# Kernel tuning notes

Hardware: AMD Instinct MI355X
Metric: run time of the kernel (lower is better)

## Reference

```python
import jax, jax.numpy as jnp
import numpy as np

B, S, D, H = 8, 1024, 512, 8
DK = D // H
NEG = -1e30  # stands in for -inf; masked probs are zero-filled afterwards, so math matches


def setup_inputs() -> dict:
    rng = jax.random.key(0)
    ks = jax.random.split(rng, 12)
    f = lambda k, shape: jax.random.normal(k, shape, dtype=jnp.float32)
    w = lambda k: f(k, (D, D)) * 0.02  # stored as (in, out); y = x @ W + b
    return {
        "query": f(ks[0], (B, S, D)),
        "key": f(ks[1], (B, S, D)),
        "value": f(ks[2], (B, S, D)),
        "mask": jax.random.randint(ks[3], (B, 1, S), 0, 2, dtype=jnp.int32),
        "Wq": w(ks[4]), "bq": jnp.zeros((D,), jnp.float32),
        "Wk": w(ks[5]), "bk": jnp.zeros((D,), jnp.float32),
        "Wv": w(ks[6]), "bv": jnp.zeros((D,), jnp.float32),
        "Wo": w(ks[7]), "bo": jnp.zeros((D,), jnp.float32),
    }


def reference(query, key, value, mask, Wq, bq, Wk, bk, Wv, bv, Wo, bo):
    # QKV projections -> (B, H, S, DK)
    def proj(x, W, b):
        return (x @ W + b).reshape(B, -1, H, DK).transpose(0, 2, 1, 3)

    q = proj(query, Wq, bq)
    k = proj(key, Wk, bk)
    v = proj(value, Wv, bv)

    scores = jnp.einsum("bhqd,bhkd->bhqk", q, k) / jnp.sqrt(jnp.float32(DK))
    m = (mask[:, None, :, :] == 0)  # (B, 1, 1, S): True where masked out
    scores = jnp.where(m, NEG, scores)
    attn = jax.nn.softmax(scores, axis=-1)
    attn = jnp.where(m, 0.0, attn)  # dropout rate is 0.0 -> identity

    x = jnp.einsum("bhqk,bhkd->bhqd", attn, v)
    x = x.transpose(0, 2, 1, 3).reshape(B, -1, D)  # (B, S, D)
    return x @ Wo + bo
```

## Files before the change

### kernel.cpp

```cpp
#include <hip/hip_runtime.h>
#include <hip/hip_bf16.h>

#define NB 8
#define NS 1024
#define ND 512
#define NH 8
#define NDK 64

typedef __attribute__((ext_vector_type(8))) short bf16x8;
typedef __attribute__((ext_vector_type(4))) float f32x4;
typedef __attribute__((ext_vector_type(16))) float f32x16;

#define QSCALE 0.18033688011112042f
#define NEGBIG -3.0e38f

#define CVTPK(dst, a, b) \
    asm("v_cvt_pk_bf16_f32 %0, %1, %2" : "=v"(dst) : "v"(a), "v"(b))
#define PLSWAP(a, b) \
    asm("v_permlane32_swap_b32 %0, %1" : "+v"(a), "+v"(b))

__device__ __forceinline__ unsigned short bfround(float f) {
    union { float f; unsigned u; } v; v.f = f;
    unsigned u = v.u;
    u += 0x7fffu + ((u >> 16) & 1u);
    return (unsigned short)(u >> 16);
}


__global__ __launch_bounds__(256) void wt_kernel(const float* __restrict__ W0,
                                                 const float* __restrict__ W1,
                                                 const float* __restrict__ W2,
                                                 const float* __restrict__ W3,
                                                 unsigned short* __restrict__ wt) {
    __shared__ float sh[64][65];
    const int z = blockIdx.z;
    const float* W = z == 0 ? W0 : z == 1 ? W1 : z == 2 ? W2 : W3;
    unsigned short* out = wt + (size_t)z * ND * ND;
    const int o0 = blockIdx.x * 64, i0 = blockIdx.y * 64;
    const int tx = threadIdx.x & 63;
    const int ty = threadIdx.x >> 6;
    #pragma unroll
    for (int rr = 0; rr < 16; ++rr) {
        const int row = ty * 16 + rr;
        sh[row][tx] = W[(size_t)(i0 + row) * ND + o0 + tx];
    }
    __syncthreads();
    #pragma unroll
    for (int rr = 0; rr < 16; ++rr) {
        const int row = ty * 16 + rr;
        out[(size_t)(o0 + row) * ND + i0 + tx] = bfround(sh[tx][row]);
    }
}

__global__ __launch_bounds__(256, 5) void gemm_qkv(
    const float* __restrict__ A0, const float* __restrict__ A1, const float* __restrict__ A2,
    const unsigned short* __restrict__ wt,
    const float* __restrict__ b0, const float* __restrict__ b1, const float* __restrict__ b2,
    unsigned short* __restrict__ outb) {
    __shared__ unsigned short SM[15360];
    const int t = threadIdx.x;
    const int lane = t & 63, w = t >> 6;
    const int wr = w >> 1, wc = w & 1;
    const int lr = lane & 15, lg = lane >> 4;
    const int bid = blockIdx.x;
    const int u = (bid & 7) * 192 + (bid >> 3);
    const int xt = u & 3, yt = (u >> 2) & 127, z = u >> 9;
    const float* A = z == 0 ? A0 : z == 1 ? A1 : A2;
    const float* bias = z == 0 ? b0 : z == 1 ? b1 : b2;
    const unsigned short* Wt = wt + (size_t)z * ND * ND;
    unsigned short* outp = outb + (size_t)z * NB * NH * NS * NDK;
    const int m0 = yt * 64, n0 = xt * 128;

    const int a_row = t >> 3;
    const int a_col = (t & 7) * 4;
    const int b_row = t >> 2;
    const int b_col = (t & 3) * 8;

    f32x4 acc[2][4];
    #pragma unroll
    for (int i = 0; i < 2; ++i)
        #pragma unroll
        for (int j = 0; j < 4; ++j) acc[i][j] = (f32x4){0.f, 0.f, 0.f, 0.f};

    f32x4 ra[2];
    bf16x8 rbv[2];

#define QKV_LOAD(kt) do {                                                      \
        const int _k0 = (kt) * 32;                                             \
        ra[0] = *(const f32x4*)(A + (size_t)(m0 + a_row) * ND + _k0 + a_col);  \
        ra[1] = *(const f32x4*)(A + (size_t)(m0 + a_row + 32) * ND + _k0 + a_col); \
        rbv[0] = *(const bf16x8*)(Wt + (size_t)(n0 + b_row) * ND + _k0 + b_col); \
        rbv[1] = *(const bf16x8*)(Wt + (size_t)(n0 + b_row + 64) * ND + _k0 + b_col); \
    } while (0)

#define QKV_WRITE(p) do {                                                      \
        _Pragma("unroll")                                                      \
        for (int j = 0; j < 2; ++j) {                                          \
            unsigned c0, c1;                                                   \
            CVTPK(c0, ra[j][0], ra[j][1]);                                     \
            CVTPK(c1, ra[j][2], ra[j][3]);                                     \
            uint2 pv; pv.x = c0; pv.y = c1;                                    \
            *(uint2*)(&SM[(p) * 2560 + (a_row + j * 32) * 40 + a_col]) = pv;   \
        }                                                                      \
        _Pragma("unroll")                                                      \
        for (int j = 0; j < 2; ++j)                                            \
            *(bf16x8*)(&SM[5120 + (p) * 5120 + (b_row + j * 64) * 40 + b_col]) = rbv[j]; \
    } while (0)

#define QKV_COMPUTE(p) do {                                                    \
        bf16x8 af[2], bfr[4];                                                  \
        _Pragma("unroll")                                                      \
        for (int mi = 0; mi < 2; ++mi)                                         \
            af[mi] = *(const bf16x8*)(&SM[(p) * 2560 + (wr * 32 + mi * 16 + lr) * 40 + lg * 8]); \
        _Pragma("unroll")                                                      \
        for (int nj = 0; nj < 4; ++nj)                                         \
            bfr[nj] = *(const bf16x8*)(&SM[5120 + (p) * 5120 + (wc * 64 + nj * 16 + lr) * 40 + lg * 8]); \
        __builtin_amdgcn_s_setprio(1);                                         \
        _Pragma("unroll")                                                      \
        for (int mi = 0; mi < 2; ++mi)                                         \
            _Pragma("unroll")                                                  \
            for (int nj = 0; nj < 4; ++nj)                                     \
                acc[mi][nj] = __builtin_amdgcn_mfma_f32_16x16x32_bf16(         \
                    af[mi], bfr[nj], acc[mi][nj], 0, 0, 0);                    \
        __builtin_amdgcn_s_setprio(0);                                         \
    } while (0)

    QKV_LOAD(0);
    QKV_WRITE(0);
    QKV_LOAD(1);
    __syncthreads();
    #pragma unroll 1
    for (int kt = 0; kt < 15; ++kt) {
        QKV_COMPUTE(kt & 1);
        QKV_WRITE((kt + 1) & 1);
        if (kt < 14) QKV_LOAD(kt + 2);
        __syncthreads();
    }
    QKV_COMPUTE(1);
#undef QKV_LOAD
#undef QKV_WRITE
#undef QKV_COMPUTE

    __syncthreads();
    const float osc = z == 0 ? QSCALE : 1.0f;
    const int bb = m0 >> 10;
    char* const C = (char*)SM;
    if (z <= 1) {
        #pragma unroll
        for (int mi = 0; mi < 2; ++mi)
            #pragma unroll
            for (int nj = 0; nj < 4; ++nj) {
                const int coln = wc * 64 + nj * 16 + lr;
                const float bv = bias[n0 + coln];
                #pragma unroll
                for (int r = 0; r < 4; ++r) {
                    const int row = wr * 32 + mi * 16 + lg * 4 + r;
                    unsigned off = (unsigned)(row * 256 + coln * 2);
                    off ^= (row & 7) << 4;
                    *(unsigned short*)(C + off) = bfround((acc[mi][nj][r] + bv) * osc);
                }
            }
        __syncthreads();
        const unsigned cb = ((unsigned)(m0 & 1023) >> 5) * 4;
        #pragma unroll
        for (int cc = 0; cc < 4; ++cc) {
            const int c = w * 4 + cc;
            const int sub = c >> 3, hhl = (c >> 2) & 1, kk = c & 3;
            const int row = sub * 32 + (lane & 31);
            unsigned off = (unsigned)(row * 256 + (hhl * 64 + kk * 16 + (lane >> 5) * 8) * 2);
            off ^= (row & 7) << 4;
            const bf16x8 v8 = *(const bf16x8*)(C + off);
            const int hh = xt * 2 + hhl;
            *(bf16x8*)(outp + (((size_t)(bb * NH + hh)) << 16) +
                       (size_t)(cb + sub * 4 + kk) * 512 + lane * 8) = v8;
        }
    } else {
        #pragma unroll
        for (int mi = 0; mi < 2; ++mi)
            #pragma unroll
            for (int nj = 0; nj < 4; ++nj) {
                const int dkl = wc * 64 + nj * 16 + lr;
                const float bv = bias[n0 + dkl];
                #pragma unroll
                for (int r = 0; r < 4; ++r) {
                    const int sl = wr * 32 + mi * 16 + lg * 4 + r;
                    unsigned off = (unsigned)(dkl * 128 + sl * 2);
                    off ^= (dkl & 7) << 4;
                    *(unsigned short*)(C + off) = bfround(acc[mi][nj][r] + bv);
                }
            }
        __syncthreads();
        const unsigned it8 = ((unsigned)(m0 & 1023) >> 6) * 8;
        #pragma unroll
        for (int cc = 0; cc < 4; ++cc) {
            const int c = w * 4 + cc;
            const int hhl = c >> 3, od = (c >> 2) & 1, s4 = c & 3;
            const int row = hhl * 64 + od * 32 + (lane & 31);
            unsigned off = (unsigned)(row * 128 + (s4 * 16 + (lane >> 5) * 8) * 2);
            off ^= (row & 7) << 4;
            const bf16x8 v8 = *(const bf16x8*)(C + off);
            const int hh = xt * 2 + hhl;
            *(bf16x8*)(outp + (((size_t)(bb * NH + hh)) << 16) +
                       (size_t)(it8 + od * 4 + s4) * 512 + lane * 8) = v8;
        }
    }
}

__global__ __launch_bounds__(256) void gemm_out(
    const unsigned short* __restrict__ Xb, const unsigned short* __restrict__ Wt,
    const float* __restrict__ bo, float* __restrict__ outp) {
    __shared__ unsigned short SM2[10240];
    const int t = threadIdx.x;
    const int lane = t & 63, w = t >> 6;
    const int wr = w >> 1, wc = w & 1;
    const int lr = lane & 15, lg = lane >> 4;
    const int bid = blockIdx.x;
    const int u = (bid & 7) * 128 + (bid >> 3);
    const int xt = u & 7, yt = u >> 3;
    const int m0 = yt * 64, n0 = xt * 64;

    const int s_row = t >> 2;
    const int s_col = (t & 3) * 8;

    f32x4 acc[2][2];
    #pragma unroll
    for (int i = 0; i < 2; ++i)
        #pragma unroll
        for (int j = 0; j < 2; ++j) acc[i][j] = (f32x4){0.f, 0.f, 0.f, 0.f};

    bf16x8 raa, rbb;

#define OUT_LOAD(kt) do {                                                      \
        const int _k0 = (kt) * 32;                                             \
        raa = *(const bf16x8*)(Xb + (size_t)(m0 + s_row) * ND + _k0 + s_col);  \
        rbb = *(const bf16x8*)(Wt + (size_t)(n0 + s_row) * ND + _k0 + s_col);  \
    } while (0)

#define OUT_WRITE(p) do {                                                      \
        *(bf16x8*)(&SM2[(p) * 2560 + s_row * 40 + s_col]) = raa;               \
        *(bf16x8*)(&SM2[5120 + (p) * 2560 + s_row * 40 + s_col]) = rbb;        \
    } while (0)

#define OUT_COMPUTE(p) do {                                                    \
        bf16x8 af[2], bfr[2];                                                  \
        _Pragma("unroll")                                                      \
        for (int mi = 0; mi < 2; ++mi)                                         \
            af[mi] = *(const bf16x8*)(&SM2[(p) * 2560 + (wr * 32 + mi * 16 + lr) * 40 + lg * 8]); \
        _Pragma("unroll")                                                      \
        for (int nj = 0; nj < 2; ++nj)                                         \
            bfr[nj] = *(const bf16x8*)(&SM2[5120 + (p) * 2560 + (wc * 32 + nj * 16 + lr) * 40 + lg * 8]); \
        __builtin_amdgcn_s_setprio(1);                                         \
        _Pragma("unroll")                                                      \
        for (int mi = 0; mi < 2; ++mi)                                         \
            _Pragma("unroll")                                                  \
            for (int nj = 0; nj < 2; ++nj)                                     \
                acc[mi][nj] = __builtin_amdgcn_mfma_f32_16x16x32_bf16(         \
                    af[mi], bfr[nj], acc[mi][nj], 0, 0, 0);                    \
        __builtin_amdgcn_s_setprio(0);                                         \
    } while (0)

    OUT_LOAD(0);
    OUT_WRITE(0);
    OUT_LOAD(1);
    __syncthreads();
    #pragma unroll 1
    for (int kt = 0; kt < 15; ++kt) {
        OUT_COMPUTE(kt & 1);
        OUT_WRITE((kt + 1) & 1);
        if (kt < 14) OUT_LOAD(kt + 2);
        __syncthreads();
    }
    OUT_COMPUTE(1);
#undef OUT_LOAD
#undef OUT_WRITE
#undef OUT_COMPUTE

    #pragma unroll
    for (int mi = 0; mi < 2; ++mi) {
        #pragma unroll
        for (int nj = 0; nj < 2; ++nj) {
            const int n = n0 + wc * 32 + nj * 16 + lr;
            const float bv = bo[n];
            #pragma unroll
            for (int r = 0; r < 4; ++r) {
                const int m = m0 + wr * 32 + mi * 16 + lg * 4 + r;
                outp[(size_t)m * ND + n] = acc[mi][nj][r] + bv;
            }
        }
    }
}

struct AttnState {
    f32x16 acc0, acc1;
    float m_st, l_st;
};

__device__ __forceinline__ void attn_step(const bf16x8 (&kf)[8], const bf16x8 (&vv)[8],
                                          const bf16x8 (&qf)[4], int mval,
                                          float* __restrict__ brow, int lane, int hi,
                                          AttnState& st) {
    brow[lane] = mval ? 0.f : NEGBIG;

    f32x16 sc0 = {}, sc1 = {};
    __builtin_amdgcn_s_setprio(1);
    sc0 = __builtin_amdgcn_mfma_f32_32x32x16_bf16(kf[0], qf[0], sc0, 0, 0, 0);
    sc1 = __builtin_amdgcn_mfma_f32_32x32x16_bf16(kf[4], qf[0], sc1, 0, 0, 0);
    sc0 = __builtin_amdgcn_mfma_f32_32x32x16_bf16(kf[1], qf[1], sc0, 0, 0, 0);
    sc1 = __builtin_amdgcn_mfma_f32_32x32x16_bf16(kf[5], qf[1], sc1, 0, 0, 0);
    sc0 = __builtin_amdgcn_mfma_f32_32x32x16_bf16(kf[2], qf[2], sc0, 0, 0, 0);
    sc1 = __builtin_amdgcn_mfma_f32_32x32x16_bf16(kf[6], qf[2], sc1, 0, 0, 0);
    sc0 = __builtin_amdgcn_mfma_f32_32x32x16_bf16(kf[3], qf[3], sc0, 0, 0, 0);
    sc1 = __builtin_amdgcn_mfma_f32_32x32x16_bf16(kf[7], qf[3], sc1, 0, 0, 0);
    __builtin_amdgcn_s_setprio(0);

    {
        const float* bl = brow + 4 * hi;
        #pragma unroll
        for (int mm = 0; mm < 4; ++mm) {
            const f32x4 bv0 = *(const f32x4*)(bl + 8 * mm);
            const f32x4 bv1 = *(const f32x4*)(bl + 32 + 8 * mm);
            #pragma unroll
            for (int c = 0; c < 4; ++c) {
                sc0[4 * mm + c] += bv0[c];
                sc1[4 * mm + c] += bv1[c];
            }
        }
    }

    float tv[16];
    #pragma unroll
    for (int r = 0; r < 16; ++r) tv[r] = fmaxf(sc0[r], sc1[r]);
    #pragma unroll
    for (int s = 8; s > 0; s >>= 1)
        #pragma unroll
        for (int r = 0; r < 16; ++r)
            if (r < s) tv[r] = fmaxf(tv[r], tv[r + s]);
    const float mx = fmaxf(tv[0], __shfl_xor(tv[0], 32));
    const float mn = fmaxf(st.m_st, mx);

    #pragma unroll
    for (int r = 0; r < 16; ++r) {
        sc0[r] = __builtin_amdgcn_exp2f(sc0[r] - mn);
        sc1[r] = __builtin_amdgcn_exp2f(sc1[r] - mn);
    }
    #pragma unroll
    for (int r = 0; r < 16; ++r) tv[r] = sc0[r] + sc1[r];
    #pragma unroll
    for (int s = 8; s > 0; s >>= 1)
        #pragma unroll
        for (int r = 0; r < 16; ++r)
            if (r < s) tv[r] += tv[r + s];
    const float rs = tv[0] + __shfl_xor(tv[0], 32);

    const bool ch = mn > st.m_st;
    if (__any(ch)) {
        const float f = __builtin_amdgcn_exp2f(st.m_st - mn);
        st.l_st = st.l_st * f + rs;
        st.m_st = mn;
        #pragma unroll
        for (int r = 0; r < 16; ++r) { st.acc0[r] *= f; st.acc1[r] *= f; }
    } else {
        st.l_st += rs;
    }

    union U8 { unsigned u[4]; bf16x8 v; };
    bf16x8 pA0, pA1, pB0, pB1;
    {
        unsigned w00, w01, w10, w11, w20, w21, w30, w31;
        CVTPK(w00, sc0[0], sc0[1]);  CVTPK(w01, sc0[2], sc0[3]);
        CVTPK(w10, sc0[4], sc0[5]);  CVTPK(w11, sc0[6], sc0[7]);
        CVTPK(w20, sc0[8], sc0[9]);  CVTPK(w21, sc0[10], sc0[11]);
        CVTPK(w30, sc0[12], sc0[13]); CVTPK(w31, sc0[14], sc0[15]);
        PLSWAP(w00, w10); PLSWAP(w01, w11);
        PLSWAP(w20, w30); PLSWAP(w21, w31);
        U8 f0; f0.u[0] = w00; f0.u[1] = w01; f0.u[2] = w10; f0.u[3] = w11;
        U8 f1; f1.u[0] = w20; f1.u[1] = w21; f1.u[2] = w30; f1.u[3] = w31;
        pA0 = f0.v; pA1 = f1.v;
    }
    {
        unsigned w00, w01, w10, w11, w20, w21, w30, w31;
        CVTPK(w00, sc1[0], sc1[1]);  CVTPK(w01, sc1[2], sc1[3]);
        CVTPK(w10, sc1[4], sc1[5]);  CVTPK(w11, sc1[6], sc1[7]);
        CVTPK(w20, sc1[8], sc1[9]);  CVTPK(w21, sc1[10], sc1[11]);
        CVTPK(w30, sc1[12], sc1[13]); CVTPK(w31, sc1[14], sc1[15]);
        PLSWAP(w00, w10); PLSWAP(w01, w11);
        PLSWAP(w20, w30); PLSWAP(w21, w31);
        U8 f0; f0.u[0] = w00; f0.u[1] = w01; f0.u[2] = w10; f0.u[3] = w11;
        U8 f1; f1.u[0] = w20; f1.u[1] = w21; f1.u[2] = w30; f1.u[3] = w31;
        pB0 = f0.v; pB1 = f1.v;
    }

    __builtin_amdgcn_s_setprio(1);
    st.acc0 = __builtin_amdgcn_mfma_f32_32x32x16_bf16(vv[0], pA0, st.acc0, 0, 0, 0);
    st.acc1 = __builtin_amdgcn_mfma_f32_32x32x16_bf16(vv[4], pA0, st.acc1, 0, 0, 0);
    st.acc0 = __builtin_amdgcn_mfma_f32_32x32x16_bf16(vv[1], pA1, st.acc0, 0, 0, 0);
    st.acc1 = __builtin_amdgcn_mfma_f32_32x32x16_bf16(vv[5], pA1, st.acc1, 0, 0, 0);
    st.acc0 = __builtin_amdgcn_mfma_f32_32x32x16_bf16(vv[2], pB0, st.acc0, 0, 0, 0);
    st.acc1 = __builtin_amdgcn_mfma_f32_32x32x16_bf16(vv[6], pB0, st.acc1, 0, 0, 0);
    st.acc0 = __builtin_amdgcn_mfma_f32_32x32x16_bf16(vv[3], pB1, st.acc0, 0, 0, 0);
    st.acc1 = __builtin_amdgcn_mfma_f32_32x32x16_bf16(vv[7], pB1, st.acc1, 0, 0, 0);
    __builtin_amdgcn_s_setprio(0);
}

__global__ __launch_bounds__(256, 2) void attn_kernel(const unsigned short* __restrict__ QF,
                                                      const unsigned short* __restrict__ KF,
                                                      const unsigned short* __restrict__ VF,
                                                      const int* __restrict__ mask,
                                                      unsigned short* __restrict__ Xb) {
    __shared__ float bias_lds[4][64];
    const int t = threadIdx.x;
    const int lane = t & 63, w = t >> 6;
    const int q32 = lane & 31, hi = lane >> 5;
    const int bid = blockIdx.x;
    const int u = (bid & 7) * 64 + (bid >> 3);
    const int bh = u >> 3, xq = u & 7;
    const int b = bh >> 3, h = bh & 7;
    const int q = xq * 128 + w * 32 + q32;
    const unsigned short* QFh = QF + ((size_t)bh << 16);
    const unsigned short* KFh = KF + ((size_t)bh << 16);
    const unsigned short* VFh = VF + ((size_t)bh << 16);
    const int* mk = mask + b * NS;
    float* brow = &bias_lds[w][0];

    bf16x8 qf[4];
    {
        const unsigned short* Qp = QFh + (size_t)(xq * 16 + w * 4) * 512 + lane * 8;
        qf[0] = *(const bf16x8*)(Qp + 0 * 512);
        qf[1] = *(const bf16x8*)(Qp + 1 * 512);
        qf[2] = *(const bf16x8*)(Qp + 2 * 512);
        qf[3] = *(const bf16x8*)(Qp + 3 * 512);
    }

    AttnState st;
    st.acc0 = (f32x16){}; st.acc1 = (f32x16){};
    st.m_st = -1.0e30f; st.l_st = 0.f;

    bf16x8 kA[8], kB[8], vv[8];

#define LOADK(dst, itx) do {                                                   \
        const unsigned short* _p = KFh + (size_t)(itx) * 4096 + lane * 8;      \
        dst[0] = *(const bf16x8*)(_p + 0 * 512);                               \
        dst[1] = *(const bf16x8*)(_p + 1 * 512);                               \
        dst[2] = *(const bf16x8*)(_p + 2 * 512);                               \
        dst[3] = *(const bf16x8*)(_p + 3 * 512);                               \
        dst[4] = *(const bf16x8*)(_p + 4 * 512);                               \
        dst[5] = *(const bf16x8*)(_p + 5 * 512);                               \
        dst[6] = *(const bf16x8*)(_p + 6 * 512);                               \
        dst[7] = *(const bf16x8*)(_p + 7 * 512);                               \
    } while (0)

#define LOADV(dst, itx) do {                                                   \
        const unsigned short* _p = VFh + (size_t)(itx) * 4096 + lane * 8;      \
        dst[0] = *(const bf16x8*)(_p + 0 * 512);                               \
        dst[1] = *(const bf16x8*)(_p + 1 * 512);                               \
        dst[2] = *(const bf16x8*)(_p + 2 * 512);                               \
        dst[3] = *(const bf16x8*)(_p + 3 * 512);                               \
        dst[4] = *(const bf16x8*)(_p + 4 * 512);                               \
        dst[5] = *(const bf16x8*)(_p + 5 * 512);                               \
        dst[6] = *(const bf16x8*)(_p + 6 * 512);                               \
        dst[7] = *(const bf16x8*)(_p + 7 * 512);                               \
    } while (0)

    LOADK(kA, 0);
    #pragma unroll 1
    for (int ii = 0; ii < 8; ++ii) {
        const int itE = ii * 2, itO = itE + 1;
        const int mE = mk[itE * 64 + lane];
        LOADV(vv, itE);
        LOADK(kB, itO);
        __builtin_amdgcn_sched_barrier(0);
        attn_step(kA, vv, qf, mE, brow, lane, hi, st);
        const int mO = mk[itO * 64 + lane];
        const int itN = itO + 1 > 15 ? 15 : itO + 1;
        LOADV(vv, itO);
        LOADK(kA, itN);
        __builtin_amdgcn_sched_barrier(0);
        attn_step(kB, vv, qf, mO, brow, lane, hi, st);
    }
#undef LOADK
#undef LOADV

    const float inv = st.l_st > 0.f ? 1.f / st.l_st : 0.f;
    unsigned short* Xp = Xb + (size_t)(b * NS + q) * ND + h * 64 + 4 * hi;
    #pragma unroll
    for (int mm = 0; mm < 4; ++mm) {
        unsigned w0, w1;
        CVTPK(w0, st.acc0[4 * mm] * inv, st.acc0[4 * mm + 1] * inv);
        CVTPK(w1, st.acc0[4 * mm + 2] * inv, st.acc0[4 * mm + 3] * inv);
        uint2 pv; pv.x = w0; pv.y = w1;
        *(uint2*)(Xp + 8 * mm) = pv;
        CVTPK(w0, st.acc1[4 * mm] * inv, st.acc1[4 * mm + 1] * inv);
        CVTPK(w1, st.acc1[4 * mm + 2] * inv, st.acc1[4 * mm + 3] * inv);
        pv.x = w0; pv.y = w1;
        *(uint2*)(Xp + 32 + 8 * mm) = pv;
    }
}

extern "C" void kernel_launch(void* const* d_in, const int* in_sizes, int n_in,
                              void* d_out, int out_size, void* d_ws, size_t ws_size,
                              hipStream_t stream) {
    const float* query = (const float*)d_in[0];
    const float* key   = (const float*)d_in[1];
    const float* value = (const float*)d_in[2];
    const int*   mask  = (const int*)d_in[3];
    const float* Wq = (const float*)d_in[4];
    const float* bq = (const float*)d_in[5];
    const float* Wk = (const float*)d_in[6];
    const float* bk = (const float*)d_in[7];
    const float* Wv = (const float*)d_in[8];
    const float* bv = (const float*)d_in[9];
    const float* Wo = (const float*)d_in[10];
    const float* bo = (const float*)d_in[11];

    const size_t HEADSZ = (size_t)NB * NH * NS * NDK;
    unsigned short* wt = (unsigned short*)d_ws;
    unsigned short* QFb = wt + (size_t)4 * ND * ND;
    unsigned short* KFb = QFb + HEADSZ;
    unsigned short* VFb = KFb + HEADSZ;
    unsigned short* Xb  = VFb + HEADSZ;

    wt_kernel<<<dim3(8, 8, 4), 256, 0, stream>>>(Wq, Wk, Wv, Wo, wt);

    gemm_qkv<<<1536, 256, 0, stream>>>(query, key, value, wt, bq, bk, bv, QFb);

    attn_kernel<<<512, 256, 0, stream>>>(QFb, KFb, VFb, mask, Xb);

    gemm_out<<<1024, 256, 0, stream>>>(Xb, wt + (size_t)3 * ND * ND, bo, (float*)d_out);
}
```

Before: 80.47 us.

## Enlarge QKV GEMM tiles to 128x128 with 64-wide K steps

```diff
diff --git a/kernel.cpp b/kernel.cpp
--- a/kernel.cpp
+++ b/kernel.cpp
@@ -52,156 +52,178 @@
     }
 }
 
-__global__ __launch_bounds__(256, 5) void gemm_qkv(
+__global__ __launch_bounds__(256) void gemm_qkv(
     const float* __restrict__ A0, const float* __restrict__ A1, const float* __restrict__ A2,
     const unsigned short* __restrict__ wt,
     const float* __restrict__ b0, const float* __restrict__ b1, const float* __restrict__ b2,
     unsigned short* __restrict__ outb) {
-    __shared__ unsigned short SM[15360];
+    __shared__ unsigned short SM[27648];
     const int t = threadIdx.x;
     const int lane = t & 63, w = t >> 6;
     const int wr = w >> 1, wc = w & 1;
     const int lr = lane & 15, lg = lane >> 4;
     const int bid = blockIdx.x;
-    const int u = (bid & 7) * 192 + (bid >> 3);
-    const int xt = u & 3, yt = (u >> 2) & 127, z = u >> 9;
+    const int u = (bid & 7) * 32 + (bid >> 3);
+    const int xt = u & 3, yt = u >> 2;
+    const int z = blockIdx.y;
     const float* A = z == 0 ? A0 : z == 1 ? A1 : A2;
     const float* bias = z == 0 ? b0 : z == 1 ? b1 : b2;
     const unsigned short* Wt = wt + (size_t)z * ND * ND;
     unsigned short* outp = outb + (size_t)z * NB * NH * NS * NDK;
-    const int m0 = yt * 64, n0 = xt * 128;
-
-    const int a_row = t >> 3;
-    const int a_col = (t & 7) * 4;
-    const int b_row = t >> 2;
-    const int b_col = (t & 3) * 8;
-
-    f32x4 acc[2][4];
-    #pragma unroll
-    for (int i = 0; i < 2; ++i)
+    const int m0 = yt * 128, n0 = xt * 128;
+
+    const int a_row = t >> 4;
+    const int a_col = (t & 15) * 4;
+    const int b_row = t >> 3;
+    const int b_col = (t & 7) * 8;
+
+    f32x4 acc[4][4];
+    #pragma unroll
+    for (int i = 0; i < 4; ++i)
         #pragma unroll
         for (int j = 0; j < 4; ++j) acc[i][j] = (f32x4){0.f, 0.f, 0.f, 0.f};
 
-    f32x4 ra[2];
-    bf16x8 rbv[2];
+    f32x4 ra[8];
+    bf16x8 rbv[4];
+
+#define AL(p) (SM + (p) * 9216)
+#define BLS (SM + 18432)
 
 #define QKV_LOAD(kt) do {                                                      \
-        const int _k0 = (kt) * 32;                                             \
-        ra[0] = *(const f32x4*)(A + (size_t)(m0 + a_row) * ND + _k0 + a_col);  \
-        ra[1] = *(const f32x4*)(A + (size_t)(m0 + a_row + 32) * ND + _k0 + a_col); \
-        rbv[0] = *(const bf16x8*)(Wt + (size_t)(n0 + b_row) * ND + _k0 + b_col); \
-        rbv[1] = *(const bf16x8*)(Wt + (size_t)(n0 + b_row + 64) * ND + _k0 + b_col); \
-    } while (0)
-
-#define QKV_WRITE(p) do {                                                      \
-        _Pragma("unroll")                                                      \
-        for (int j = 0; j < 2; ++j) {                                          \
+        const int _k0 = (kt) * 64;                                             \
+        _Pragma("unroll")                                                      \
+        for (int j = 0; j < 8; ++j)                                            \
+            ra[j] = *(const f32x4*)(A + (size_t)(m0 + a_row + j * 16) * ND + _k0 + a_col); \
+        _Pragma("unroll")                                                      \
+        for (int j = 0; j < 4; ++j)                                            \
+            rbv[j] = *(const bf16x8*)(Wt + (size_t)(n0 + b_row + j * 32) * ND + _k0 + b_col); \
+    } while (0)
+
+#define QKV_WRITEA(p) do {                                                     \
+        _Pragma("unroll")                                                      \
+        for (int j = 0; j < 8; ++j) {                                          \
             unsigned c0, c1;                                                   \
             CVTPK(c0, ra[j][0], ra[j][1]);                                     \
             CVTPK(c1, ra[j][2], ra[j][3]);                                     \
             uint2 pv; pv.x = c0; pv.y = c1;                                    \
-            *(uint2*)(&SM[(p) * 2560 + (a_row + j * 32) * 40 + a_col]) = pv;   \
+            *(uint2*)(&AL(p)[(a_row + j * 16) * 72 + a_col]) = pv;             \
         }                                                                      \
-        _Pragma("unroll")                                                      \
-        for (int j = 0; j < 2; ++j)                                            \
-            *(bf16x8*)(&SM[5120 + (p) * 5120 + (b_row + j * 64) * 40 + b_col]) = rbv[j]; \
+    } while (0)
+
+#define QKV_WRITEB() do {                                                      \
+        _Pragma("unroll")                                                      \
+        for (int j = 0; j < 4; ++j)                                            \
+            *(bf16x8*)(&BLS[(b_row + j * 32) * 72 + b_col]) = rbv[j];          \
     } while (0)
 
 #define QKV_COMPUTE(p) do {                                                    \
-        bf16x8 af[2], bfr[4];                                                  \
-        _Pragma("unroll")                                                      \
-        for (int mi = 0; mi < 2; ++mi)                                         \
-            af[mi] = *(const bf16x8*)(&SM[(p) * 2560 + (wr * 32 + mi * 16 + lr) * 40 + lg * 8]); \
-        _Pragma("unroll")                                                      \
-        for (int nj = 0; nj < 4; ++nj)                                         \
-            bfr[nj] = *(const bf16x8*)(&SM[5120 + (p) * 5120 + (wc * 64 + nj * 16 + lr) * 40 + lg * 8]); \
-        __builtin_amdgcn_s_setprio(1);                                         \
-        _Pragma("unroll")                                                      \
-        for (int mi = 0; mi < 2; ++mi)                                         \
+        _Pragma("unroll")                                                      \
+        for (int kk = 0; kk < 2; ++kk) {                                       \
+            bf16x8 af[4], bfr[4];                                              \
+            _Pragma("unroll")                                                  \
+            for (int mi = 0; mi < 4; ++mi)                                     \
+                af[mi] = *(const bf16x8*)(&AL(p)[(wr * 64 + mi * 16 + lr) * 72 + kk * 32 + lg * 8]); \
             _Pragma("unroll")                                                  \
             for (int nj = 0; nj < 4; ++nj)                                     \
-                acc[mi][nj] = __builtin_amdgcn_mfma_f32_16x16x32_bf16(         \
-                    af[mi], bfr[nj], acc[mi][nj], 0, 0, 0);                    \
-        __builtin_amdgcn_s_setprio(0);                                         \
+                bfr[nj] = *(const bf16x8*)(&BLS[(wc * 64 + nj * 16 + lr) * 72 + kk * 32 + lg * 8]); \
+            __builtin_amdgcn_s_setprio(1);                                     \
+            _Pragma("unroll")                                                  \
+            for (int mi = 0; mi < 4; ++mi)                                     \
+                _Pragma("unroll")                                              \
+                for (int nj = 0; nj < 4; ++nj)                                 \
+                    acc[mi][nj] = __builtin_amdgcn_mfma_f32_16x16x32_bf16(     \
+                        af[mi], bfr[nj], acc[mi][nj], 0, 0, 0);                \
+            __builtin_amdgcn_s_setprio(0);                                     \
+        }                                                                      \
     } while (0)
 
     QKV_LOAD(0);
-    QKV_WRITE(0);
+    QKV_WRITEA(0);
+    QKV_WRITEB();
     QKV_LOAD(1);
+    __builtin_amdgcn_sched_barrier(0);
     __syncthreads();
     #pragma unroll 1
-    for (int kt = 0; kt < 15; ++kt) {
+    for (int kt = 0; kt < 7; ++kt) {
         QKV_COMPUTE(kt & 1);
-        QKV_WRITE((kt + 1) & 1);
-        if (kt < 14) QKV_LOAD(kt + 2);
+        __syncthreads();
+        QKV_WRITEA((kt + 1) & 1);
+        QKV_WRITEB();
+        QKV_LOAD(kt + 2 > 7 ? 7 : kt + 2);
+        __builtin_amdgcn_sched_barrier(0);
         __syncthreads();
     }
     QKV_COMPUTE(1);
 #undef QKV_LOAD
-#undef QKV_WRITE
+#undef QKV_WRITEA
+#undef QKV_WRITEB
 #undef QKV_COMPUTE
+#undef AL
+#undef BLS
 
     __syncthreads();
     const float osc = z == 0 ? QSCALE : 1.0f;
     const int bb = m0 >> 10;
+    const unsigned msb = (unsigned)(m0 & 1023);
     char* const C = (char*)SM;
     if (z <= 1) {
         #pragma unroll
-        for (int mi = 0; mi < 2; ++mi)
+        for (int mi = 0; mi < 4; ++mi)
             #pragma unroll
             for (int nj = 0; nj < 4; ++nj) {
                 const int coln = wc * 64 + nj * 16 + lr;
                 const float bv = bias[n0 + coln];
                 #pragma unroll
                 for (int r = 0; r < 4; ++r) {
-                    const int row = wr * 32 + mi * 16 + lg * 4 + r;
+                    const int row = wr * 64 + mi * 16 + lg * 4 + r;
                     unsigned off = (unsigned)(row * 256 + coln * 2);
                     off ^= (row & 7) << 4;
                     *(unsigned short*)(C + off) = bfround((acc[mi][nj][r] + bv) * osc);
                 }
             }
         __syncthreads();
-        const unsigned cb = ((unsigned)(m0 & 1023) >> 5) * 4;
-        #pragma unroll
-        for (int cc = 0; cc < 4; ++cc) {
-            const int c = w * 4 + cc;
-            const int sub = c >> 3, hhl = (c >> 2) & 1, kk = c & 3;
-            const int row = sub * 32 + (lane & 31);
+        #pragma unroll
+        for (int cc = 0; cc < 8; ++cc) {
+            const int c = w * 8 + cc;
+            const int sg = c >> 3, hhl = (c >> 2) & 1, kk = c & 3;
+            const int row = sg * 32 + (lane & 31);
             unsigned off = (unsigned)(row * 256 + (hhl * 64 + kk * 16 + (lane >> 5) * 8) * 2);
             off ^= (row & 7) << 4;
             const bf16x8 v8 = *(const bf16x8*)(C + off);
             const int hh = xt * 2 + hhl;
+            const unsigned chunk = z == 0 ? ((msb >> 5) + sg) * 4 + kk
+                                          : ((msb >> 6) + (sg >> 1)) * 8 + (sg & 1) * 4 + kk;
             *(bf16x8*)(outp + (((size_t)(bb * NH + hh)) << 16) +
-                       (size_t)(cb + sub * 4 + kk) * 512 + lane * 8) = v8;
+                       (size_t)chunk * 512 + lane * 8) = v8;
         }
     } else {
         #pragma unroll
-        for (int mi = 0; mi < 2; ++mi)
+        for (int mi = 0; mi < 4; ++mi)
             #pragma unroll
             for (int nj = 0; nj < 4; ++nj) {
                 const int dkl = wc * 64 + nj * 16 + lr;
                 const float bv = bias[n0 + dkl];
                 #pragma unroll
                 for (int r = 0; r < 4; ++r) {
-                    const int sl = wr * 32 + mi * 16 + lg * 4 + r;
-                    unsigned off = (unsigned)(dkl * 128 + sl * 2);
+                    const int sl = wr * 64 + mi * 16 + lg * 4 + r;
+                    unsigned off = (unsigned)(dkl * 256 + sl * 2);
                     off ^= (dkl & 7) << 4;
                     *(unsigned short*)(C + off) = bfround(acc[mi][nj][r] + bv);
                 }
             }
         __syncthreads();
-        const unsigned it8 = ((unsigned)(m0 & 1023) >> 6) * 8;
-        #pragma unroll
-        for (int cc = 0; cc < 4; ++cc) {
-            const int c = w * 4 + cc;
-            const int hhl = c >> 3, od = (c >> 2) & 1, s4 = c & 3;
+        #pragma unroll
+        for (int cc = 0; cc < 8; ++cc) {
+            const int c = w * 8 + cc;
+            const int hhl = c >> 4, s6 = (c >> 3) & 1, od = (c >> 2) & 1, s4 = c & 3;
             const int row = hhl * 64 + od * 32 + (lane & 31);
-            unsigned off = (unsigned)(row * 128 + (s4 * 16 + (lane >> 5) * 8) * 2);
+            unsigned off = (unsigned)(row * 256 + (s6 * 64 + s4 * 16 + (lane >> 5) * 8) * 2);
             off ^= (row & 7) << 4;
             const bf16x8 v8 = *(const bf16x8*)(C + off);
             const int hh = xt * 2 + hhl;
+            const unsigned chunk = ((msb >> 6) + s6) * 8 + od * 4 + s4;
             *(bf16x8*)(outp + (((size_t)(bb * NH + hh)) << 16) +
-                       (size_t)(it8 + od * 4 + s4) * 512 + lane * 8) = v8;
+                       (size_t)chunk * 512 + lane * 8) = v8;
         }
     }
 }
@@ -521,7 +543,7 @@
 
     wt_kernel<<<dim3(8, 8, 4), 256, 0, stream>>>(Wq, Wk, Wv, Wo, wt);
 
-    gemm_qkv<<<1536, 256, 0, stream>>>(query, key, value, wt, bq, bk, bv, QFb);
+    gemm_qkv<<<dim3(256, 3), 256, 0, stream>>>(query, key, value, wt, bq, bk, bv, QFb);
 
     attn_kernel<<<512, 256, 0, stream>>>(QFb, KFb, VFb, mask, Xb);
 
```

New measurement: 77.76 us, median of 2. 1.03x faster.
